# Performance work log

Hardware: AMD Instinct MI355X
Metric: run time of the kernel (lower is better)

Reference implementation:

```python
import jax, jax.numpy as jnp
import numpy as np

D = 1024
H = 16
HD = D // H  # 64
S = 2048
B = 1


def setup_inputs() -> dict:
    key = jax.random.key(0)
    ks = jax.random.split(key, 6)
    return {
        "GLO": jax.random.normal(ks[0], (B, S, D), dtype=jnp.float32),
        "LOC": jax.random.normal(ks[1], (B, S, D), dtype=jnp.float32),
        "W_q": jax.random.normal(ks[2], (H, D, HD), dtype=jnp.float32),
        "W_k": jax.random.normal(ks[3], (H, D, HD), dtype=jnp.float32),
        "W_v": jax.random.normal(ks[4], (H, D, HD), dtype=jnp.float32),
        "W_o": jax.random.normal(ks[5], (H * HD, D), dtype=jnp.float32),
    }


def _cross_attn(q_src, kv_src, W_q, W_k, W_v, W_o):
    # q_src: [B,Sq,D], kv_src: [B,Sk,D]
    b, sq, _ = q_src.shape
    Q = jnp.einsum('bsd,hde->bhse', q_src, W_q)   # [B,H,Sq,hd]
    K = jnp.einsum('bsd,hde->bhse', kv_src, W_k)  # [B,H,Sk,hd]
    V = jnp.einsum('bsd,hde->bhse', kv_src, W_v)  # [B,H,Sk,hd]
    scores = jnp.einsum('bhqe,bhke->bhqk', Q, K) / jnp.sqrt(jnp.float32(HD))
    weights = jax.nn.softmax(scores, axis=-1)
    out = jnp.einsum('bhqk,bhke->bhqe', weights, V)  # [B,H,Sq,hd]
    # Faithful to torch .view (raw memory reinterpretation, no head transpose)
    out = out.reshape(b, sq, H * HD)
    return out @ W_o  # [B,Sq,D]


def reference(GLO, LOC, W_q, W_k, W_v, W_o):
    GLO_prime = _cross_attn(GLO, LOC, W_q, W_k, W_v, W_o)
    LOC_prime = _cross_attn(LOC, GLO, W_q, W_k, W_v, W_o)
    return (GLO_prime, LOC_prime)
```

## Files before the change

### kernel.cpp

```cpp
#include <hip/hip_runtime.h>
#include <math.h>

#define S_LEN 2048
#define D_DIM 1024
#define NH 16
#define HD 64

typedef __attribute__((ext_vector_type(8))) short bf16x8;
typedef __attribute__((ext_vector_type(4))) float f32x4;

#define MFMA(a, b, c) __builtin_amdgcn_mfma_f32_16x16x32_bf16((a), (b), (c), 0, 0, 0)

__device__ __forceinline__ unsigned short f2bf(float x) {
    unsigned int u = __float_as_uint(x);
    u = (u + 0x7FFFu + ((u >> 16) & 1u)) >> 16;
    return (unsigned short)u;
}
__device__ __forceinline__ float bf2f(unsigned short b) {
    return __uint_as_float(((unsigned int)b) << 16);
}
__device__ __forceinline__ void gl_lds16(const void* g, void* l) {
    __builtin_amdgcn_global_load_lds((const __attribute__((address_space(1))) unsigned int*)g,
                                     (__attribute__((address_space(3))) unsigned int*)l, 16, 0, 0);
}

#if defined(__has_builtin)
#if __has_builtin(__builtin_amdgcn_cvt_pk_bf16_f32)
#define HAVE_CVT_PK_BF16 1
#endif
#endif
__device__ __forceinline__ unsigned pack_bf16(float a, float b) {
#ifdef HAVE_CVT_PK_BF16
    auto r = __builtin_amdgcn_cvt_pk_bf16_f32(a, b);
    unsigned u;
    __builtin_memcpy(&u, &r, 4);
    return u;
#else
    unsigned ua = __float_as_uint(a) + 0x8000u;
    unsigned ub = __float_as_uint(b) + 0x8000u;
    return __builtin_amdgcn_perm(ub, ua, 0x07060302u);
#endif
}


__global__ __launch_bounds__(256) void prep(const float* __restrict__ GLO,
                                            const float* __restrict__ LOC,
                                            const float* __restrict__ Wq,
                                            const float* __restrict__ Wk,
                                            const float* __restrict__ Wv,
                                            const float* __restrict__ Wo,
                                            unsigned short* __restrict__ Xh,
                                            unsigned short* __restrict__ Xl,
                                            unsigned short* __restrict__ Wqh,
                                            unsigned short* __restrict__ Wql,
                                            unsigned short* __restrict__ Wkh,
                                            unsigned short* __restrict__ Wkl,
                                            unsigned short* __restrict__ Wvt,
                                            unsigned short* __restrict__ Wot) {
    int idx = blockIdx.x * 256 + threadIdx.x;
    if (idx < (1 << 19)) {
        int gg = idx & 7;
        int row = (idx >> 3) & 127;
        int kblk = (idx >> 10) & 15;
        int r = (idx >> 14) * 128 + row;
        int kg = gg ^ (row & 7);
        const float* src = (r & 2048) ? LOC : GLO;
        const float* sp = src + (size_t)(r & 2047) * 1024 + kblk * 64 + kg * 8;
        float4 x0 = *(const float4*)sp;
        float4 x1 = *(const float4*)(sp + 4);
        size_t t = (size_t)idx * 8;
        ushort4 h0, l0, h1, l1;
        h0.x = f2bf(x0.x); l0.x = f2bf(x0.x - bf2f(h0.x));
        h0.y = f2bf(x0.y); l0.y = f2bf(x0.y - bf2f(h0.y));
        h0.z = f2bf(x0.z); l0.z = f2bf(x0.z - bf2f(h0.z));
        h0.w = f2bf(x0.w); l0.w = f2bf(x0.w - bf2f(h0.w));
        h1.x = f2bf(x1.x); l1.x = f2bf(x1.x - bf2f(h1.x));
        h1.y = f2bf(x1.y); l1.y = f2bf(x1.y - bf2f(h1.y));
        h1.z = f2bf(x1.z); l1.z = f2bf(x1.z - bf2f(h1.z));
        h1.w = f2bf(x1.w); l1.w = f2bf(x1.w - bf2f(h1.w));
        *(ushort4*)(Xh + t) = h0;
        *(ushort4*)(Xh + t + 4) = h1;
        *(ushort4*)(Xl + t) = l0;
        *(ushort4*)(Xl + t + 4) = l1;
    } else {
        int idx2 = idx - (1 << 19);
        int sec = idx2 >> 17;
        int j = idx2 & 0x1FFFF;
        size_t t = (size_t)j * 8;
        if (sec < 3) {
            int gg = j & 7;
            int e = (j >> 3) & 63;
            int kblk = (j >> 9) & 15;
            int head = j >> 13;
            int kg = gg ^ (e & 7);
            int d0 = kblk * 64 + kg * 8;
            const float* W = (sec == 0) ? Wq : (sec == 1) ? Wk : Wv;
            const float* wp = W + (size_t)head * 65536 + (size_t)d0 * 64 + e;
            float wv8[8];
#pragma unroll
            for (int i = 0; i < 8; ++i) wv8[i] = wp[i * 64];
            if (sec == 0) {
                ushort4 h0, l0, h1, l1;
#pragma unroll
                for (int i = 0; i < 8; ++i) {
                    float v = wv8[i] * 0.18033688011112042f;
                    unsigned short hi = f2bf(v);
                    unsigned short lo = f2bf(v - bf2f(hi));
                    if (i < 4) {
                        ((unsigned short*)&h0)[i] = hi;
                        ((unsigned short*)&l0)[i] = lo;
                    } else {
                        ((unsigned short*)&h1)[i - 4] = hi;
                        ((unsigned short*)&l1)[i - 4] = lo;
                    }
                }
                *(ushort4*)(Wqh + t) = h0;
                *(ushort4*)(Wqh + t + 4) = h1;
                *(ushort4*)(Wql + t) = l0;
                *(ushort4*)(Wql + t + 4) = l1;
            } else if (sec == 1) {
                ushort4 h0, l0, h1, l1;
#pragma unroll
                for (int i = 0; i < 8; ++i) {
                    float v = wv8[i];
                    unsigned short hi = f2bf(v);
                    unsigned short lo = f2bf(v - bf2f(hi));
                    if (i < 4) {
                        ((unsigned short*)&h0)[i] = hi;
                        ((unsigned short*)&l0)[i] = lo;
                    } else {
                        ((unsigned short*)&h1)[i - 4] = hi;
                        ((unsigned short*)&l1)[i - 4] = lo;
                    }
                }
                *(ushort4*)(Wkh + t) = h0;
                *(ushort4*)(Wkh + t + 4) = h1;
                *(ushort4*)(Wkl + t) = l0;
                *(ushort4*)(Wkl + t + 4) = l1;
            } else {
                ushort4 v0, v1;
#pragma unroll
                for (int i = 0; i < 8; ++i) {
                    unsigned short b = f2bf(wv8[i]);
                    if (i < 4)
                        ((unsigned short*)&v0)[i] = b;
                    else
                        ((unsigned short*)&v1)[i - 4] = b;
                }
                *(ushort4*)(Wvt + t) = v0;
                *(ushort4*)(Wvt + t + 4) = v1;
            }
        } else {
            int gg = j & 7;
            int col = (j >> 3) & 63;
            int kblk = (j >> 9) & 15;
            int nblk = j >> 13;
            int kg = gg ^ (col & 7);
            int k0 = kblk * 64 + kg * 8;
            int n = nblk * 64 + col;
            ushort4 v0, v1;
#pragma unroll
            for (int i = 0; i < 8; ++i) {
                unsigned short b = f2bf(Wo[(size_t)(k0 + i) * 1024 + n]);
                if (i < 4)
                    ((unsigned short*)&v0)[i] = b;
                else
                    ((unsigned short*)&v1)[i - 4] = b;
            }
            *(ushort4*)(Wot + t) = v0;
            *(ushort4*)(Wot + t + 4) = v1;
        }
    }
}

__global__ __launch_bounds__(256) void qkv_proj(const unsigned short* __restrict__ Xh,
                                                const unsigned short* __restrict__ Xl,
                                                const unsigned short* __restrict__ Wqh,
                                                const unsigned short* __restrict__ Wql,
                                                const unsigned short* __restrict__ Wkh,
                                                const unsigned short* __restrict__ Wkl,
                                                const unsigned short* __restrict__ Wvt,
                                                unsigned short* __restrict__ Qh,
                                                unsigned short* __restrict__ Ql,
                                                unsigned short* __restrict__ Kh,
                                                unsigned short* __restrict__ Kl,
                                                unsigned short* __restrict__ Vt) {
    __shared__ unsigned short lds[36864];
    const int bid = blockIdx.x;
    const int mblk = bid & 31;
    const int head = bid >> 5;
    const int tid = threadIdx.x;
    const int lane = tid & 63;
    const int w = tid >> 6;
    const int l15 = lane & 15, quad = lane >> 4;

    f32x4 aq[2][4] = {}, ak[2][4] = {}, av[2][4] = {};
    const size_t abase0 = (size_t)mblk * 131072;
    const size_t bbase0 = (size_t)head * 65536;

    for (int kb = 0; kb < 16; ++kb) {
        __syncthreads();
        {
            const size_t ab = abase0 + (size_t)kb * 8192;
            const size_t bb = bbase0 + (size_t)kb * 4096;
#pragma unroll
            for (int j = 0; j < 4; ++j) {
                int seg = j * 256 + tid;
                gl_lds16(Xh + ab + seg * 8, &lds[seg * 8]);
                gl_lds16(Xl + ab + seg * 8, &lds[8192 + seg * 8]);
            }
#pragma unroll
            for (int j = 0; j < 2; ++j) {
                int seg = j * 256 + tid;
                gl_lds16(Wqh + bb + seg * 8, &lds[16384 + seg * 8]);
                gl_lds16(Wql + bb + seg * 8, &lds[20480 + seg * 8]);
                gl_lds16(Wkh + bb + seg * 8, &lds[24576 + seg * 8]);
                gl_lds16(Wkl + bb + seg * 8, &lds[28672 + seg * 8]);
                gl_lds16(Wvt + bb + seg * 8, &lds[32768 + seg * 8]);
            }
        }
        __syncthreads();

#pragma unroll
        for (int ksub = 0; ksub < 2; ++ksub) {
            bf16x8 ah[2], al8[2];
#pragma unroll
            for (int mt = 0; mt < 2; ++mt) {
                int row = w * 32 + mt * 16 + l15;
                int g = (ksub * 4 + quad) ^ (row & 7);
                ah[mt] = *(const bf16x8*)&lds[row * 64 + g * 8];
                al8[mt] = *(const bf16x8*)&lds[8192 + row * 64 + g * 8];
            }
#pragma unroll
            for (int nt = 0; nt < 4; ++nt) {
                int col = nt * 16 + l15;
                int o = col * 64 + ((ksub * 4 + quad) ^ (col & 7)) * 8;
                bf16x8 bqh = *(const bf16x8*)&lds[16384 + o];
                bf16x8 bql = *(const bf16x8*)&lds[20480 + o];
                bf16x8 bkh = *(const bf16x8*)&lds[24576 + o];
                bf16x8 bkl = *(const bf16x8*)&lds[28672 + o];
                bf16x8 bv = *(const bf16x8*)&lds[32768 + o];
#pragma unroll
                for (int mt = 0; mt < 2; ++mt) {
                    f32x4 a = aq[mt][nt];
                    a = MFMA(ah[mt], bqh, a);
                    a = MFMA(ah[mt], bql, a);
                    a = MFMA(al8[mt], bqh, a);
                    aq[mt][nt] = a;
                    f32x4 b = ak[mt][nt];
                    b = MFMA(ah[mt], bkh, b);
                    b = MFMA(ah[mt], bkl, b);
                    b = MFMA(al8[mt], bkh, b);
                    ak[mt][nt] = b;
                    av[mt][nt] = MFMA(ah[mt], bv, av[mt][nt]);
                }
            }
        }
    }

#pragma unroll
    for (int mt = 0; mt < 2; ++mt) {
        const int rbase = mblk * 128 + w * 32 + mt * 16 + quad * 4;
#pragma unroll
        for (int nt = 0; nt < 4; ++nt) {
            const int col = head * 64 + nt * 16 + l15;
#pragma unroll
            for (int r = 0; r < 4; ++r) {
                size_t a = (size_t)(rbase + r) * D_DIM + col;
                float vq = aq[mt][nt][r];
                unsigned short hq = f2bf(vq);
                Qh[a] = hq;
                Ql[a] = f2bf(vq - bf2f(hq));
                float vk = ak[mt][nt][r];
                unsigned short hk = f2bf(vk);
                Kh[a] = hk;
                Kl[a] = f2bf(vk - bf2f(hk));
            }
            ushort4 vp;
            vp.x = f2bf(av[mt][nt][0]);
            vp.y = f2bf(av[mt][nt][1]);
            vp.z = f2bf(av[mt][nt][2]);
            vp.w = f2bf(av[mt][nt][3]);
            *(ushort4*)(Vt + (size_t)col * (2 * S_LEN) + rbase) = vp;
        }
    }
}

__global__ __launch_bounds__(256) void attn_kernel(const unsigned short* __restrict__ Qh_,
                                                   const unsigned short* __restrict__ Ql_,
                                                   const unsigned short* __restrict__ Kh_,
                                                   const unsigned short* __restrict__ Kl_,
                                                   const unsigned short* __restrict__ Vt_,
                                                   unsigned short* __restrict__ Oatt) {
    __shared__ unsigned short lds[28672];
    const int bid = blockIdx.x;
    const int qblk = bid & 15;
    const int head = (bid >> 4) & 15;
    const int dir = bid >> 8;
    const int src_q = dir, src_kv = 1 - dir;

    const int tid = threadIdx.x;
    const int lane = tid & 63;
    const int w = tid >> 6;
    const int l15 = lane & 15, quad = lane >> 4;
    const int q0w = qblk * 128 + w * 32;

    const unsigned short* KhB0 = Kh_ + (size_t)(src_kv * S_LEN) * D_DIM + head * 64;
    const unsigned short* KlB0 = Kl_ + (size_t)(src_kv * S_LEN) * D_DIM + head * 64;
    const unsigned short* Vtp = Vt_ + (size_t)(head * 64) * (2 * S_LEN) + src_kv * S_LEN;

    const int i0 = tid, i1 = 256 + tid;
    const int sr0 = i0 >> 3, sc0 = ((i0 & 7) ^ (sr0 & 7)) * 8;
    const int sr1 = i1 >> 3, sc1 = ((i1 & 7) ^ (sr1 & 7)) * 8;

    auto stage = [&](int k0, int boff) {
        const unsigned short* KhB = KhB0 + (size_t)k0 * D_DIM;
        const unsigned short* KlB = KlB0 + (size_t)k0 * D_DIM;
        const unsigned short* VB = Vtp + k0;
        gl_lds16(KhB + (size_t)sr0 * D_DIM + sc0, &lds[boff + i0 * 8]);
        gl_lds16(KhB + (size_t)sr1 * D_DIM + sc1, &lds[boff + i1 * 8]);
        gl_lds16(KlB + (size_t)sr0 * D_DIM + sc0, &lds[boff + 4096 + i0 * 8]);
        gl_lds16(KlB + (size_t)sr1 * D_DIM + sc1, &lds[boff + 4096 + i1 * 8]);
        gl_lds16(VB + (size_t)sr0 * (2 * S_LEN) + sc0, &lds[boff + 8192 + i0 * 8]);
        gl_lds16(VB + (size_t)sr1 * (2 * S_LEN) + sc1, &lds[boff + 8192 + i1 * 8]);
    };

    bf16x8 qh[2][2], ql[2][2];
#pragma unroll
    for (int mt = 0; mt < 2; ++mt) {
        const size_t qrow =
            (size_t)(src_q * S_LEN + q0w + mt * 16 + l15) * D_DIM + head * 64 + quad * 8;
#pragma unroll
        for (int c = 0; c < 2; ++c) {
            qh[mt][c] = *(const bf16x8*)(Qh_ + qrow + c * 32);
            ql[mt][c] = *(const bf16x8*)(Ql_ + qrow + c * 32);
        }
    }

    f32x4 o[2][4] = {};
    float mi[2] = {-1e30f, -1e30f};
    float lip[2] = {0.f, 0.f};
    unsigned short* Pw = lds + 24576 + w * 1024;

    auto chunk = [&](int kb) {
        f32x4 sa[2][4];
#pragma unroll
        for (int kt = 0; kt < 4; ++kt) {
            const int row = kt * 16 + l15;
            const int s0 = (quad ^ (row & 7)) * 8;
            const int s1 = ((4 + quad) ^ (row & 7)) * 8;
            bf16x8 kh0 = *(const bf16x8*)&lds[kb + row * 64 + s0];
            bf16x8 kh1 = *(const bf16x8*)&lds[kb + row * 64 + s1];
            bf16x8 kl0 = *(const bf16x8*)&lds[kb + 4096 + row * 64 + s0];
            bf16x8 kl1 = *(const bf16x8*)&lds[kb + 4096 + row * 64 + s1];
#pragma unroll
            for (int mt = 0; mt < 2; ++mt) {
                f32x4 a = {};
                a = MFMA(kh0, qh[mt][0], a);
                a = MFMA(kh1, qh[mt][1], a);
                a = MFMA(kl0, qh[mt][0], a);
                a = MFMA(kl1, qh[mt][1], a);
                a = MFMA(kh0, ql[mt][0], a);
                a = MFMA(kh1, ql[mt][1], a);
                sa[mt][kt] = a;
            }
        }

#pragma unroll
        for (int mt = 0; mt < 2; ++mt) {
            f32x4 t4 = __builtin_elementwise_max(__builtin_elementwise_max(sa[mt][0], sa[mt][1]),
                                                 __builtin_elementwise_max(sa[mt][2], sa[mt][3]));
            float tm = fmaxf(fmaxf(t4[0], t4[1]), fmaxf(t4[2], t4[3]));
            tm = fmaxf(tm, __shfl_xor(tm, 16, 64));
            tm = fmaxf(tm, __shfl_xor(tm, 32, 64));
            if (__ballot(tm > mi[mt])) {
                float mn = fmaxf(mi[mt], tm);
                float al = exp2f(mi[mt] - mn);
                mi[mt] = mn;
                lip[mt] *= al;
                const f32x4 alv = {al, al, al, al};
#pragma unroll
                for (int et = 0; et < 4; ++et) o[mt][et] *= alv;
            }
            const float mn = mi[mt];
            const f32x4 mnv = {mn, mn, mn, mn};
            f32x4 rs4 = {};
#pragma unroll
            for (int kt = 0; kt < 4; ++kt) {
                f32x4 p = sa[mt][kt] - mnv;
#pragma unroll
                for (int r = 0; r < 4; ++r) p[r] = exp2f(p[r]);
                rs4 += p;
                uint2 pk;
                pk.x = pack_bf16(p[0], p[1]);
                pk.y = pack_bf16(p[2], p[3]);
                int g = (kt * 2 + (quad >> 1)) ^ (l15 & 7);
                *(uint2*)&Pw[l15 * 64 + g * 8 + (quad & 1) * 4] = pk;
            }
            lip[mt] += (rs4[0] + rs4[1]) + (rs4[2] + rs4[3]);

#pragma unroll
            for (int c = 0; c < 2; ++c) {
                bf16x8 pf = *(const bf16x8*)&Pw[l15 * 64 + (((c * 4 + quad) ^ (l15 & 7)) * 8)];
#pragma unroll
                for (int et = 0; et < 4; ++et) {
                    const int row = et * 16 + l15;
                    const int sl = ((c * 4 + quad) ^ (row & 7)) * 8;
                    bf16x8 vf = *(const bf16x8*)&lds[kb + 8192 + row * 64 + sl];
                    o[mt][et] = MFMA(vf, pf, o[mt][et]);
                }
            }
        }
    };

    stage(0, 0);
#pragma unroll 1
    for (int kd = 0; kd < 32; kd += 2) {
        __syncthreads();
        if (kd + 1 < 32) stage((kd + 1) * 64, 12288);
        chunk(0);
        __syncthreads();
        if (kd + 2 < 32) stage((kd + 2) * 64, 0);
        chunk(12288);
    }

    const size_t obase = (size_t)(dir * 16 + head) * 131072 + (size_t)l15 * 8192;
#pragma unroll
    for (int mt = 0; mt < 2; ++mt) {
        float lq = lip[mt];
        lq += __shfl_xor(lq, 16, 64);
        lq += __shfl_xor(lq, 32, 64);
        float rl = __builtin_amdgcn_rcpf(lq);
        const int rowit = qblk * 8 + w * 2 + mt;
#pragma unroll
        for (int et = 0; et < 4; ++et) {
            int g = ((et * 2 + (quad >> 1)) ^ (rowit & 7)) & 7;
            ushort4 pk;
            pk.x = f2bf(o[mt][et][0] * rl);
            pk.y = f2bf(o[mt][et][1] * rl);
            pk.z = f2bf(o[mt][et][2] * rl);
            pk.w = f2bf(o[mt][et][3] * rl);
            *(ushort4*)(Oatt + obase + (size_t)rowit * 64 + g * 8 + (quad & 1) * 4) = pk;
        }
    }
}

__global__ __launch_bounds__(256) void oproj(const unsigned short* __restrict__ Oatt,
                                             const unsigned short* __restrict__ Wot,
                                             float* __restrict__ out) {
    __shared__ unsigned short lds[24576];
    const int bid = blockIdx.x;
    const int nblk = bid & 15;
    const int mblk = bid >> 4;
    const int tid = threadIdx.x;
    const int lane = tid & 63, w = tid >> 6, l15 = lane & 15, quad = lane >> 4;

    f32x4 acc[2][4] = {};
    const size_t abase = (size_t)mblk * 131072;
    const size_t bbase = (size_t)nblk * 65536;

    auto ostage = [&](int kb, int boff) {
#pragma unroll
        for (int j = 0; j < 4; ++j) {
            int seg = j * 256 + tid;
            gl_lds16(Oatt + abase + (size_t)kb * 8192 + seg * 8, &lds[boff + seg * 8]);
        }
#pragma unroll
        for (int j = 0; j < 2; ++j) {
            int seg = j * 256 + tid;
            gl_lds16(Wot + bbase + (size_t)kb * 4096 + seg * 8, &lds[boff + 8192 + seg * 8]);
        }
    };

    auto compute = [&](int boff) {
#pragma unroll
        for (int ksub = 0; ksub < 2; ++ksub) {
            bf16x8 a[2];
#pragma unroll
            for (int mt = 0; mt < 2; ++mt) {
                int row = w * 32 + mt * 16 + l15;
                a[mt] =
                    *(const bf16x8*)&lds[boff + row * 64 + (((ksub * 4 + quad) ^ (row & 7)) * 8)];
            }
#pragma unroll
            for (int nt = 0; nt < 4; ++nt) {
                int col = nt * 16 + l15;
                bf16x8 b = *(const bf16x8*)&lds[boff + 8192 + col * 64 +
                                                (((ksub * 4 + quad) ^ (col & 7)) * 8)];
#pragma unroll
                for (int mt = 0; mt < 2; ++mt) acc[mt][nt] = MFMA(a[mt], b, acc[mt][nt]);
            }
        }
    };

    ostage(0, 0);
#pragma unroll 1
    for (int kb = 0; kb < 16; kb += 2) {
        __syncthreads();
        if (kb + 1 < 16) ostage(kb + 1, 12288);
        compute(0);
        __syncthreads();
        if (kb + 2 < 16) ostage(kb + 2, 0);
        compute(12288);
    }

#pragma unroll
    for (int mt = 0; mt < 2; ++mt) {
        const int rbase = mblk * 128 + w * 32 + mt * 16 + quad * 4;
#pragma unroll
        for (int nt = 0; nt < 4; ++nt)
#pragma unroll
            for (int r = 0; r < 4; ++r)
                out[(size_t)(rbase + r) * D_DIM + nblk * 64 + nt * 16 + l15] = acc[mt][nt][r];
    }
}

extern "C" void kernel_launch(void* const* d_in, const int* in_sizes, int n_in, void* d_out,
                              int out_size, void* d_ws, size_t ws_size, hipStream_t stream) {
    const float* GLO = (const float*)d_in[0];
    const float* LOC = (const float*)d_in[1];
    const float* Wq = (const float*)d_in[2];
    const float* Wk = (const float*)d_in[3];
    const float* Wv = (const float*)d_in[4];
    const float* Wo = (const float*)d_in[5];
    float* out = (float*)d_out;

    unsigned short* ws = (unsigned short*)d_ws;
    unsigned short* Xh = ws + 0;
    unsigned short* Xl = ws + 4194304;
    unsigned short* Wqh = ws + 8388608;
    unsigned short* Wql = ws + 9437184;
    unsigned short* Wkh = ws + 10485760;
    unsigned short* Wkl = ws + 11534336;
    unsigned short* Wvt = ws + 12582912;
    unsigned short* Wot = ws + 13631488;
    unsigned short* Qh = ws + 14680064;
    unsigned short* Ql = ws + 18874368;
    unsigned short* Kh = ws + 23068672;
    unsigned short* Kl = ws + 27262976;
    unsigned short* Vt = ws + 31457280;
    unsigned short* Oatt = ws + 35651584;

    prep<<<4096, 256, 0, stream>>>(GLO, LOC, Wq, Wk, Wv, Wo, Xh, Xl, Wqh, Wql, Wkh, Wkl, Wvt, Wot);
    qkv_proj<<<512, 256, 0, stream>>>(Xh, Xl, Wqh, Wql, Wkh, Wkl, Wvt, Qh, Ql, Kh, Kl, Vt);
    attn_kernel<<<512, 256, 0, stream>>>(Qh, Ql, Kh, Kl, Vt, Oatt);
    oproj<<<512, 256, 0, stream>>>(Oatt, Wot, out);
}
```

Before: 246.2 us.

## Use 8 waves per attention block with one 16-row tile each, row-sum via MFMA

Attention blocks now launch 512 threads (8 waves), with each wave owning a single 16-query tile instead of two, so each thread issues half as many K/V staging loads. The softmax row sum is now accumulated by an MFMA against a vector of bf16 ones, replacing the per-lane exp sums and the shuffle reductions. LDS grows to hold eight per-wave P buffers. This trades per-wave register work for more waves per CU and more latency hiding. The risk is occupancy limits from the larger LDS footprint, and row sums now taken over bf16-rounded probabilities.

```diff
diff --git a/kernel.cpp b/kernel.cpp
--- a/kernel.cpp
+++ b/kernel.cpp
@@ -286,13 +286,13 @@
     }
 }
 
-__global__ __launch_bounds__(256) void attn_kernel(const unsigned short* __restrict__ Qh_,
-                                                   const unsigned short* __restrict__ Ql_,
-                                                   const unsigned short* __restrict__ Kh_,
-                                                   const unsigned short* __restrict__ Kl_,
-                                                   const unsigned short* __restrict__ Vt_,
-                                                   unsigned short* __restrict__ Oatt) {
-    __shared__ unsigned short lds[28672];
+__global__ __launch_bounds__(512, 4) void attn_kernel(const unsigned short* __restrict__ Qh_,
+                                                      const unsigned short* __restrict__ Ql_,
+                                                      const unsigned short* __restrict__ Kh_,
+                                                      const unsigned short* __restrict__ Kl_,
+                                                      const unsigned short* __restrict__ Vt_,
+                                                      unsigned short* __restrict__ Oatt) {
+    __shared__ unsigned short lds[32768];
     const int bid = blockIdx.x;
     const int qblk = bid & 15;
     const int head = (bid >> 4) & 15;
@@ -303,47 +303,45 @@
     const int lane = tid & 63;
     const int w = tid >> 6;
     const int l15 = lane & 15, quad = lane >> 4;
-    const int q0w = qblk * 128 + w * 32;
+    const int q0w = qblk * 128 + w * 16;
 
     const unsigned short* KhB0 = Kh_ + (size_t)(src_kv * S_LEN) * D_DIM + head * 64;
     const unsigned short* KlB0 = Kl_ + (size_t)(src_kv * S_LEN) * D_DIM + head * 64;
     const unsigned short* Vtp = Vt_ + (size_t)(head * 64) * (2 * S_LEN) + src_kv * S_LEN;
 
-    const int i0 = tid, i1 = 256 + tid;
+    const int i0 = tid;
     const int sr0 = i0 >> 3, sc0 = ((i0 & 7) ^ (sr0 & 7)) * 8;
-    const int sr1 = i1 >> 3, sc1 = ((i1 & 7) ^ (sr1 & 7)) * 8;
 
     auto stage = [&](int k0, int boff) {
         const unsigned short* KhB = KhB0 + (size_t)k0 * D_DIM;
         const unsigned short* KlB = KlB0 + (size_t)k0 * D_DIM;
         const unsigned short* VB = Vtp + k0;
         gl_lds16(KhB + (size_t)sr0 * D_DIM + sc0, &lds[boff + i0 * 8]);
-        gl_lds16(KhB + (size_t)sr1 * D_DIM + sc1, &lds[boff + i1 * 8]);
         gl_lds16(KlB + (size_t)sr0 * D_DIM + sc0, &lds[boff + 4096 + i0 * 8]);
-        gl_lds16(KlB + (size_t)sr1 * D_DIM + sc1, &lds[boff + 4096 + i1 * 8]);
         gl_lds16(VB + (size_t)sr0 * (2 * S_LEN) + sc0, &lds[boff + 8192 + i0 * 8]);
-        gl_lds16(VB + (size_t)sr1 * (2 * S_LEN) + sc1, &lds[boff + 8192 + i1 * 8]);
     };
 
-    bf16x8 qh[2][2], ql[2][2];
-#pragma unroll
-    for (int mt = 0; mt < 2; ++mt) {
-        const size_t qrow =
-            (size_t)(src_q * S_LEN + q0w + mt * 16 + l15) * D_DIM + head * 64 + quad * 8;
+    bf16x8 qh[2], ql[2];
+    {
+        const size_t qrow = (size_t)(src_q * S_LEN + q0w + l15) * D_DIM + head * 64 + quad * 8;
 #pragma unroll
         for (int c = 0; c < 2; ++c) {
-            qh[mt][c] = *(const bf16x8*)(Qh_ + qrow + c * 32);
-            ql[mt][c] = *(const bf16x8*)(Ql_ + qrow + c * 32);
-        }
-    }
-
-    f32x4 o[2][4] = {};
-    float mi[2] = {-1e30f, -1e30f};
-    float lip[2] = {0.f, 0.f};
+            qh[c] = *(const bf16x8*)(Qh_ + qrow + c * 32);
+            ql[c] = *(const bf16x8*)(Ql_ + qrow + c * 32);
+        }
+    }
+
+    bf16x8 ones_;
+#pragma unroll
+    for (int i = 0; i < 8; ++i) ones_[i] = (short)0x3F80;
+
+    f32x4 o[4] = {};
+    f32x4 li = {};
+    float mi = -1e30f;
     unsigned short* Pw = lds + 24576 + w * 1024;
 
     auto chunk = [&](int kb) {
-        f32x4 sa[2][4];
+        f32x4 sa[4];
 #pragma unroll
         for (int kt = 0; kt < 4; ++kt) {
             const int row = kt * 16 + l15;
@@ -353,62 +351,53 @@
             bf16x8 kh1 = *(const bf16x8*)&lds[kb + row * 64 + s1];
             bf16x8 kl0 = *(const bf16x8*)&lds[kb + 4096 + row * 64 + s0];
             bf16x8 kl1 = *(const bf16x8*)&lds[kb + 4096 + row * 64 + s1];
-#pragma unroll
-            for (int mt = 0; mt < 2; ++mt) {
-                f32x4 a = {};
-                a = MFMA(kh0, qh[mt][0], a);
-                a = MFMA(kh1, qh[mt][1], a);
-                a = MFMA(kl0, qh[mt][0], a);
-                a = MFMA(kl1, qh[mt][1], a);
-                a = MFMA(kh0, ql[mt][0], a);
-                a = MFMA(kh1, ql[mt][1], a);
-                sa[mt][kt] = a;
-            }
-        }
-
-#pragma unroll
-        for (int mt = 0; mt < 2; ++mt) {
-            f32x4 t4 = __builtin_elementwise_max(__builtin_elementwise_max(sa[mt][0], sa[mt][1]),
-                                                 __builtin_elementwise_max(sa[mt][2], sa[mt][3]));
-            float tm = fmaxf(fmaxf(t4[0], t4[1]), fmaxf(t4[2], t4[3]));
-            tm = fmaxf(tm, __shfl_xor(tm, 16, 64));
-            tm = fmaxf(tm, __shfl_xor(tm, 32, 64));
-            if (__ballot(tm > mi[mt])) {
-                float mn = fmaxf(mi[mt], tm);
-                float al = exp2f(mi[mt] - mn);
-                mi[mt] = mn;
-                lip[mt] *= al;
-                const f32x4 alv = {al, al, al, al};
-#pragma unroll
-                for (int et = 0; et < 4; ++et) o[mt][et] *= alv;
-            }
-            const float mn = mi[mt];
-            const f32x4 mnv = {mn, mn, mn, mn};
-            f32x4 rs4 = {};
-#pragma unroll
-            for (int kt = 0; kt < 4; ++kt) {
-                f32x4 p = sa[mt][kt] - mnv;
-#pragma unroll
-                for (int r = 0; r < 4; ++r) p[r] = exp2f(p[r]);
-                rs4 += p;
-                uint2 pk;
-                pk.x = pack_bf16(p[0], p[1]);
-                pk.y = pack_bf16(p[2], p[3]);
-                int g = (kt * 2 + (quad >> 1)) ^ (l15 & 7);
-                *(uint2*)&Pw[l15 * 64 + g * 8 + (quad & 1) * 4] = pk;
-            }
-            lip[mt] += (rs4[0] + rs4[1]) + (rs4[2] + rs4[3]);
-
-#pragma unroll
-            for (int c = 0; c < 2; ++c) {
-                bf16x8 pf = *(const bf16x8*)&Pw[l15 * 64 + (((c * 4 + quad) ^ (l15 & 7)) * 8)];
-#pragma unroll
-                for (int et = 0; et < 4; ++et) {
-                    const int row = et * 16 + l15;
-                    const int sl = ((c * 4 + quad) ^ (row & 7)) * 8;
-                    bf16x8 vf = *(const bf16x8*)&lds[kb + 8192 + row * 64 + sl];
-                    o[mt][et] = MFMA(vf, pf, o[mt][et]);
-                }
+            f32x4 a = {};
+            a = MFMA(kh0, qh[0], a);
+            a = MFMA(kh1, qh[1], a);
+            a = MFMA(kl0, qh[0], a);
+            a = MFMA(kl1, qh[1], a);
+            a = MFMA(kh0, ql[0], a);
+            a = MFMA(kh1, ql[1], a);
+            sa[kt] = a;
+        }
+
+        f32x4 t4 = __builtin_elementwise_max(__builtin_elementwise_max(sa[0], sa[1]),
+                                             __builtin_elementwise_max(sa[2], sa[3]));
+        float tm = fmaxf(fmaxf(t4[0], t4[1]), fmaxf(t4[2], t4[3]));
+        tm = fmaxf(tm, __shfl_xor(tm, 16, 64));
+        tm = fmaxf(tm, __shfl_xor(tm, 32, 64));
+        if (__ballot(tm > mi)) {
+            float mn = fmaxf(mi, tm);
+            float al = exp2f(mi - mn);
+            mi = mn;
+            const f32x4 alv = {al, al, al, al};
+            li *= alv;
+#pragma unroll
+            for (int et = 0; et < 4; ++et) o[et] *= alv;
+        }
+        const f32x4 mnv = {mi, mi, mi, mi};
+#pragma unroll
+        for (int kt = 0; kt < 4; ++kt) {
+            f32x4 p = sa[kt] - mnv;
+#pragma unroll
+            for (int r = 0; r < 4; ++r) p[r] = exp2f(p[r]);
+            uint2 pk;
+            pk.x = pack_bf16(p[0], p[1]);
+            pk.y = pack_bf16(p[2], p[3]);
+            int g = (kt * 2 + (quad >> 1)) ^ (l15 & 7);
+            *(uint2*)&Pw[l15 * 64 + g * 8 + (quad & 1) * 4] = pk;
+        }
+
+#pragma unroll
+        for (int c = 0; c < 2; ++c) {
+            bf16x8 pf = *(const bf16x8*)&Pw[l15 * 64 + (((c * 4 + quad) ^ (l15 & 7)) * 8)];
+            li = MFMA(ones_, pf, li);
+#pragma unroll
+            for (int et = 0; et < 4; ++et) {
+                const int row = et * 16 + l15;
+                const int sl = ((c * 4 + quad) ^ (row & 7)) * 8;
+                bf16x8 vf = *(const bf16x8*)&lds[kb + 8192 + row * 64 + sl];
+                o[et] = MFMA(vf, pf, o[et]);
             }
         }
     };
@@ -425,21 +414,17 @@
     }
 
     const size_t obase = (size_t)(dir * 16 + head) * 131072 + (size_t)l15 * 8192;
-#pragma unroll
-    for (int mt = 0; mt < 2; ++mt) {
-        float lq = lip[mt];
-        lq += __shfl_xor(lq, 16, 64);
-        lq += __shfl_xor(lq, 32, 64);
-        float rl = __builtin_amdgcn_rcpf(lq);
-        const int rowit = qblk * 8 + w * 2 + mt;
+    {
+        float rl = __builtin_amdgcn_rcpf(li[0]);
+        const int rowit = qblk * 8 + w;
 #pragma unroll
         for (int et = 0; et < 4; ++et) {
             int g = ((et * 2 + (quad >> 1)) ^ (rowit & 7)) & 7;
             ushort4 pk;
-            pk.x = f2bf(o[mt][et][0] * rl);
-            pk.y = f2bf(o[mt][et][1] * rl);
-            pk.z = f2bf(o[mt][et][2] * rl);
-            pk.w = f2bf(o[mt][et][3] * rl);
+            pk.x = f2bf(o[et][0] * rl);
+            pk.y = f2bf(o[et][1] * rl);
+            pk.z = f2bf(o[et][2] * rl);
+            pk.w = f2bf(o[et][3] * rl);
             *(ushort4*)(Oatt + obase + (size_t)rowit * 64 + g * 8 + (quad & 1) * 4) = pk;
         }
     }
@@ -543,6 +528,6 @@
 
     prep<<<4096, 256, 0, stream>>>(GLO, LOC, Wq, Wk, Wv, Wo, Xh, Xl, Wqh, Wql, Wkh, Wkl, Wvt, Wot);
     qkv_proj<<<512, 256, 0, stream>>>(Xh, Xl, Wqh, Wql, Wkh, Wkl, Wvt, Qh, Ql, Kh, Kl, Vt);
-    attn_kernel<<<512, 256, 0, stream>>>(Qh, Ql, Kh, Kl, Vt, Oatt);
+    attn_kernel<<<512, 512, 0, stream>>>(Qh, Ql, Kh, Kl, Vt, Oatt);
     oproj<<<512, 256, 0, stream>>>(Oatt, Wot, out);
 }
```

New measurement: 246.3 us. Within noise of the previous version (+0.1%).

## Split attention over key halves with partial outputs and LSE combine kernel

Applied to the files above, without the earlier changes.

Splits each attention block's key range in two (split-K flash attention), doubling the grid to 1024 blocks. Each block writes a normalized partial output and a log-sum-exp, and a new combine kernel merges the halves into the swizzled Oatt layout. LDS drops to a single buffer so four blocks can fit per CU, and s_setprio raises wave priority around the MFMA sections. In exchange, staging is no longer overlapped with compute within a block, and the change adds an extra kernel launch, extra global traffic for the partials, and bf16 rounding of the partial outputs.

```diff
diff --git a/kernel.cpp b/kernel.cpp
--- a/kernel.cpp
+++ b/kernel.cpp
@@ -286,17 +286,19 @@
     }
 }
 
-__global__ __launch_bounds__(256) void attn_kernel(const unsigned short* __restrict__ Qh_,
-                                                   const unsigned short* __restrict__ Ql_,
-                                                   const unsigned short* __restrict__ Kh_,
-                                                   const unsigned short* __restrict__ Kl_,
-                                                   const unsigned short* __restrict__ Vt_,
-                                                   unsigned short* __restrict__ Oatt) {
-    __shared__ unsigned short lds[28672];
+__global__ __launch_bounds__(256, 4) void attn_kernel(const unsigned short* __restrict__ Qh_,
+                                                      const unsigned short* __restrict__ Ql_,
+                                                      const unsigned short* __restrict__ Kh_,
+                                                      const unsigned short* __restrict__ Kl_,
+                                                      const unsigned short* __restrict__ Vt_,
+                                                      unsigned short* __restrict__ Opart,
+                                                      float* __restrict__ Lse) {
+    __shared__ unsigned short lds[16384];
     const int bid = blockIdx.x;
     const int qblk = bid & 15;
     const int head = (bid >> 4) & 15;
-    const int dir = bid >> 8;
+    const int dir = (bid >> 8) & 1;
+    const int khalf = bid >> 9;
     const int src_q = dir, src_kv = 1 - dir;
 
     const int tid = threadIdx.x;
@@ -305,24 +307,23 @@
     const int l15 = lane & 15, quad = lane >> 4;
     const int q0w = qblk * 128 + w * 32;
 
-    const unsigned short* KhB0 = Kh_ + (size_t)(src_kv * S_LEN) * D_DIM + head * 64;
-    const unsigned short* KlB0 = Kl_ + (size_t)(src_kv * S_LEN) * D_DIM + head * 64;
-    const unsigned short* Vtp = Vt_ + (size_t)(head * 64) * (2 * S_LEN) + src_kv * S_LEN;
-
-    const int i0 = tid, i1 = 256 + tid;
-    const int sr0 = i0 >> 3, sc0 = ((i0 & 7) ^ (sr0 & 7)) * 8;
-    const int sr1 = i1 >> 3, sc1 = ((i1 & 7) ^ (sr1 & 7)) * 8;
-
-    auto stage = [&](int k0, int boff) {
-        const unsigned short* KhB = KhB0 + (size_t)k0 * D_DIM;
-        const unsigned short* KlB = KlB0 + (size_t)k0 * D_DIM;
-        const unsigned short* VB = Vtp + k0;
-        gl_lds16(KhB + (size_t)sr0 * D_DIM + sc0, &lds[boff + i0 * 8]);
-        gl_lds16(KhB + (size_t)sr1 * D_DIM + sc1, &lds[boff + i1 * 8]);
-        gl_lds16(KlB + (size_t)sr0 * D_DIM + sc0, &lds[boff + 4096 + i0 * 8]);
-        gl_lds16(KlB + (size_t)sr1 * D_DIM + sc1, &lds[boff + 4096 + i1 * 8]);
-        gl_lds16(VB + (size_t)sr0 * (2 * S_LEN) + sc0, &lds[boff + 8192 + i0 * 8]);
-        gl_lds16(VB + (size_t)sr1 * (2 * S_LEN) + sc1, &lds[boff + 8192 + i1 * 8]);
+    const unsigned short* KhB0 =
+        Kh_ + (size_t)(src_kv * S_LEN + khalf * 1024) * D_DIM + head * 64;
+    const unsigned short* KlB0 =
+        Kl_ + (size_t)(src_kv * S_LEN + khalf * 1024) * D_DIM + head * 64;
+    const unsigned short* Vtp =
+        Vt_ + (size_t)(head * 64) * (2 * S_LEN) + src_kv * S_LEN + khalf * 1024;
+
+    auto stage = [&](int k0) {
+#pragma unroll
+        for (int j = 0; j < 2; ++j) {
+            int i = j * 256 + tid;
+            int row = i >> 3;
+            int col = ((i & 7) ^ (row & 7)) * 8;
+            gl_lds16(KhB0 + (size_t)(k0 + row) * D_DIM + col, &lds[i * 8]);
+            gl_lds16(KlB0 + (size_t)(k0 + row) * D_DIM + col, &lds[4096 + i * 8]);
+            gl_lds16(Vtp + (size_t)row * (2 * S_LEN) + k0 + col, &lds[8192 + i * 8]);
+        }
     };
 
     bf16x8 qh[2][2], ql[2][2];
@@ -340,19 +341,20 @@
     f32x4 o[2][4] = {};
     float mi[2] = {-1e30f, -1e30f};
     float lip[2] = {0.f, 0.f};
-    unsigned short* Pw = lds + 24576 + w * 1024;
-
-    auto chunk = [&](int kb) {
+    unsigned short* Pw = lds + 12288 + w * 1024;
+
+    auto chunk = [&]() {
         f32x4 sa[2][4];
+        __builtin_amdgcn_s_setprio(1);
 #pragma unroll
         for (int kt = 0; kt < 4; ++kt) {
             const int row = kt * 16 + l15;
             const int s0 = (quad ^ (row & 7)) * 8;
             const int s1 = ((4 + quad) ^ (row & 7)) * 8;
-            bf16x8 kh0 = *(const bf16x8*)&lds[kb + row * 64 + s0];
-            bf16x8 kh1 = *(const bf16x8*)&lds[kb + row * 64 + s1];
-            bf16x8 kl0 = *(const bf16x8*)&lds[kb + 4096 + row * 64 + s0];
-            bf16x8 kl1 = *(const bf16x8*)&lds[kb + 4096 + row * 64 + s1];
+            bf16x8 kh0 = *(const bf16x8*)&lds[row * 64 + s0];
+            bf16x8 kh1 = *(const bf16x8*)&lds[row * 64 + s1];
+            bf16x8 kl0 = *(const bf16x8*)&lds[4096 + row * 64 + s0];
+            bf16x8 kl1 = *(const bf16x8*)&lds[4096 + row * 64 + s1];
 #pragma unroll
             for (int mt = 0; mt < 2; ++mt) {
                 f32x4 a = {};
@@ -365,6 +367,7 @@
                 sa[mt][kt] = a;
             }
         }
+        __builtin_amdgcn_s_setprio(0);
 
 #pragma unroll
         for (int mt = 0; mt < 2; ++mt) {
@@ -399,6 +402,7 @@
             }
             lip[mt] += (rs4[0] + rs4[1]) + (rs4[2] + rs4[3]);
 
+            __builtin_amdgcn_s_setprio(1);
 #pragma unroll
             for (int c = 0; c < 2; ++c) {
                 bf16x8 pf = *(const bf16x8*)&Pw[l15 * 64 + (((c * 4 + quad) ^ (l15 & 7)) * 8)];
@@ -406,43 +410,86 @@
                 for (int et = 0; et < 4; ++et) {
                     const int row = et * 16 + l15;
                     const int sl = ((c * 4 + quad) ^ (row & 7)) * 8;
-                    bf16x8 vf = *(const bf16x8*)&lds[kb + 8192 + row * 64 + sl];
+                    bf16x8 vf = *(const bf16x8*)&lds[8192 + row * 64 + sl];
                     o[mt][et] = MFMA(vf, pf, o[mt][et]);
                 }
             }
+            __builtin_amdgcn_s_setprio(0);
         }
     };
 
-    stage(0, 0);
 #pragma unroll 1
-    for (int kd = 0; kd < 32; kd += 2) {
+    for (int c = 0; c < 16; ++c) {
         __syncthreads();
-        if (kd + 1 < 32) stage((kd + 1) * 64, 12288);
-        chunk(0);
+        stage(c * 64);
         __syncthreads();
-        if (kd + 2 < 32) stage((kd + 2) * 64, 0);
-        chunk(12288);
-    }
-
-    const size_t obase = (size_t)(dir * 16 + head) * 131072 + (size_t)l15 * 8192;
+        chunk();
+    }
+
+    const size_t pbase = (size_t)(khalf * 32 + dir * 16 + head) * 2048;
 #pragma unroll
     for (int mt = 0; mt < 2; ++mt) {
         float lq = lip[mt];
         lq += __shfl_xor(lq, 16, 64);
         lq += __shfl_xor(lq, 32, 64);
-        float rl = __builtin_amdgcn_rcpf(lq);
-        const int rowit = qblk * 8 + w * 2 + mt;
+        const float rl = __builtin_amdgcn_rcpf(lq);
+        const int q = qblk * 128 + w * 32 + mt * 16 + l15;
+        const size_t ob = (pbase + q) * 64;
 #pragma unroll
         for (int et = 0; et < 4; ++et) {
-            int g = ((et * 2 + (quad >> 1)) ^ (rowit & 7)) & 7;
             ushort4 pk;
             pk.x = f2bf(o[mt][et][0] * rl);
             pk.y = f2bf(o[mt][et][1] * rl);
             pk.z = f2bf(o[mt][et][2] * rl);
             pk.w = f2bf(o[mt][et][3] * rl);
-            *(ushort4*)(Oatt + obase + (size_t)rowit * 64 + g * 8 + (quad & 1) * 4) = pk;
-        }
-    }
+            *(ushort4*)(Opart + ob + et * 16 + quad * 4) = pk;
+        }
+        if (quad == 0) Lse[pbase + q] = mi[mt] + __log2f(lq);
+    }
+}
+
+__global__ __launch_bounds__(256) void combine(const unsigned short* __restrict__ Opart,
+                                               const float* __restrict__ Lse,
+                                               unsigned short* __restrict__ Oatt) {
+    const int t = blockIdx.x * 256 + threadIdx.x;
+    const int qi = t >> 3;
+    const int e0 = (t & 7) * 8;
+    const int dh = qi >> 11;
+    const int q = qi & 2047;
+
+    const size_t row1 = (size_t)dh * 2048 + q;
+    const size_t b1 = row1 * 64 + e0;
+    const size_t b2 = b1 + (size_t)4194304;
+    ushort4 p1a = *(const ushort4*)(Opart + b1);
+    ushort4 p1b = *(const ushort4*)(Opart + b1 + 4);
+    ushort4 p2a = *(const ushort4*)(Opart + b2);
+    ushort4 p2b = *(const ushort4*)(Opart + b2 + 4);
+    const float l1 = Lse[row1];
+    const float l2 = Lse[row1 + 65536];
+
+    const float M = fmaxf(l1, l2);
+    float w1 = exp2f(l1 - M);
+    float w2 = exp2f(l2 - M);
+    const float rw = __builtin_amdgcn_rcpf(w1 + w2);
+    w1 *= rw;
+    w2 *= rw;
+
+    ushort4 oa, ob;
+    oa.x = f2bf(bf2f(p1a.x) * w1 + bf2f(p2a.x) * w2);
+    oa.y = f2bf(bf2f(p1a.y) * w1 + bf2f(p2a.y) * w2);
+    oa.z = f2bf(bf2f(p1a.z) * w1 + bf2f(p2a.z) * w2);
+    oa.w = f2bf(bf2f(p1a.w) * w1 + bf2f(p2a.w) * w2);
+    ob.x = f2bf(bf2f(p1b.x) * w1 + bf2f(p2b.x) * w2);
+    ob.y = f2bf(bf2f(p1b.y) * w1 + bf2f(p2b.y) * w2);
+    ob.z = f2bf(bf2f(p1b.z) * w1 + bf2f(p2b.z) * w2);
+    ob.w = f2bf(bf2f(p1b.w) * w1 + bf2f(p2b.w) * w2);
+
+    const int rowit = q >> 4;
+    const int g = ((e0 >> 3) ^ (rowit & 7)) & 7;
+    const size_t oaddr =
+        (size_t)dh * 131072 + (size_t)(q & 15) * 8192 + (size_t)rowit * 64 + g * 8;
+    *(ushort4*)(Oatt + oaddr) = oa;
+    *(ushort4*)(Oatt + oaddr + 4) = ob;
 }
 
 __global__ __launch_bounds__(256) void oproj(const unsigned short* __restrict__ Oatt,
@@ -540,9 +587,12 @@
     unsigned short* Kl = ws + 27262976;
     unsigned short* Vt = ws + 31457280;
     unsigned short* Oatt = ws + 35651584;
+    unsigned short* Opart = ws + 0;
+    float* LseP = (float*)(ws + 8388608);
 
     prep<<<4096, 256, 0, stream>>>(GLO, LOC, Wq, Wk, Wv, Wo, Xh, Xl, Wqh, Wql, Wkh, Wkl, Wvt, Wot);
     qkv_proj<<<512, 256, 0, stream>>>(Xh, Xl, Wqh, Wql, Wkh, Wkl, Wvt, Qh, Ql, Kh, Kl, Vt);
-    attn_kernel<<<512, 256, 0, stream>>>(Qh, Ql, Kh, Kl, Vt, Oatt);
+    attn_kernel<<<1024, 256, 0, stream>>>(Qh, Ql, Kh, Kl, Vt, Opart, LseP);
+    combine<<<2048, 256, 0, stream>>>(Opart, LseP, Oatt);
     oproj<<<512, 256, 0, stream>>>(Oatt, Wot, out);
 }
```

Result: slower. 269.7 us (+9.6%).
